# Kernel tuning notes

Measured on AMD Instinct MI355X. Metric: run time of the kernel, lower is better.

Reference implementation:

```python
import jax, jax.numpy as jnp
import numpy as np

QK_I2_S = 128  # weights per block; 32 packed bytes per block
RMS_EPS = 1e-6  # RMSNorm default eps (BitNetMLP builds RMSNorm without eps arg)


def unpack_simd(packed, K):
    """Unpack SIMD block-interleaved 2-bit weights to float {-1,0,1,2}-1 values.

    packed: [M, K//4] uint8. Within each 128-weight block (32 bytes):
      byte[j] bits 6:7 -> w[j+0], 4:5 -> w[j+32], 2:3 -> w[j+64], 0:1 -> w[j+96].
    """
    M = packed.shape[0]
    nb = K // QK_I2_S
    b = packed.astype(jnp.int32).reshape(M, nb, 32)
    # stack shift groups so flattened order is [j+0..31, j+32.., j+64.., j+96..]
    w = jnp.stack([(b >> 6) & 3, (b >> 4) & 3, (b >> 2) & 3, b & 3], axis=2)  # [M,nb,4,32]
    return w.reshape(M, K).astype(jnp.float32) - 1.0


def setup_inputs() -> dict:
    key = jax.random.key(0)
    ks = jax.random.split(key, 8)
    H, I = 2560, 6912
    B, S = 4, 2048
    x = jax.random.normal(ks[0], (B, S, H), dtype=jnp.float32)
    gate_packed = jax.random.randint(ks[1], (I, H // 4), 0, 256, dtype=jnp.int32).astype(jnp.uint8)
    up_packed = jax.random.randint(ks[2], (I, H // 4), 0, 256, dtype=jnp.int32).astype(jnp.uint8)
    down_packed = jax.random.randint(ks[3], (H, I // 4), 0, 256, dtype=jnp.int32).astype(jnp.uint8)
    gate_scale = jax.random.uniform(ks[4], (1,), minval=0.01, maxval=0.1, dtype=jnp.float32)
    up_scale = jax.random.uniform(ks[5], (1,), minval=0.01, maxval=0.1, dtype=jnp.float32)
    down_scale = jax.random.uniform(ks[6], (1,), minval=0.01, maxval=0.1, dtype=jnp.float32)
    norm_w = jnp.ones((I,), dtype=jnp.float32) + 0.05 * jax.random.normal(ks[7], (I,), dtype=jnp.float32)
    return {"x": x, "gate_packed": gate_packed, "gate_scale": gate_scale,
            "up_packed": up_packed, "up_scale": up_scale,
            "down_packed": down_packed, "down_scale": down_scale,
            "norm_w": norm_w}


def reference(x, gate_packed, gate_scale, up_packed, up_scale, down_packed, down_scale, norm_w):
    H = x.shape[-1]
    I = norm_w.shape[0]
    # BitLinear (fallback path math): unpack ternary weights, apply scalar weight scale
    Wg = unpack_simd(gate_packed, H) * gate_scale[0]   # [I, H]
    Wu = unpack_simd(up_packed, H) * up_scale[0]       # [I, H]
    Wd = unpack_simd(down_packed, I) * down_scale[0]   # [H, I]
    gate = jnp.einsum('bsh,ih->bsi', x, Wg)
    up = jnp.einsum('bsh,ih->bsi', x, Wu)
    hidden = jnp.square(jax.nn.relu(gate)) * up        # ReLU^2 gating
    # RMSNorm over intermediate dim
    var = jnp.mean(jnp.square(hidden), axis=-1, keepdims=True)
    hidden = norm_w * (hidden * jax.lax.rsqrt(var + RMS_EPS))
    return jnp.einsum('bsi,hi->bsh', hidden, Wd)
```

## Files before the change

### kernel.cpp

```cpp
#include <hip/hip_runtime.h>
#include <cstdint>
#include <cstddef>

#define H_DIM 2560
#define I_DIM 6912
#define NTOK  8192

typedef __attribute__((ext_vector_type(8))) __bf16 bf16x8;
typedef __attribute__((ext_vector_type(4))) float  f32x4;

__device__ inline void gld16(void* lds, const void* g) {
    __builtin_amdgcn_global_load_lds(
        (__attribute__((address_space(1))) void*)(void*)g,
        (__attribute__((address_space(3))) void*)lds, 16, 0, 0);
}

__global__ __launch_bounds__(256) void cvt_x_kernel(const float* __restrict__ x,
                                                    __bf16* __restrict__ xb, int n8) {
    int gid = blockIdx.x * 256 + threadIdx.x;
    if (gid >= n8) return;
    const float4* p = (const float4*)(x + (size_t)gid * 8);
    float4 v0 = p[0], v1 = p[1];
    bf16x8 o;
    o[0] = (__bf16)v0.x; o[1] = (__bf16)v0.y; o[2] = (__bf16)v0.z; o[3] = (__bf16)v0.w;
    o[4] = (__bf16)v1.x; o[5] = (__bf16)v1.y; o[6] = (__bf16)v1.z; o[7] = (__bf16)v1.w;
    *(bf16x8*)(xb + (size_t)gid * 8) = o;
}

__global__ __launch_bounds__(256) void unpack_w_kernel(const int* __restrict__ packed,
                                                       __bf16* __restrict__ out,
                                                       int M, int K,
                                                       const float* __restrict__ norm,
                                                       int mode) {
    int gid = blockIdx.x * 256 + threadIdx.x;
    int per_row = K >> 3;
    if (gid >= M * per_row) return;
    int i  = gid / per_row;
    int k0 = (gid % per_row) * 8;
    int blk = k0 >> 7;
    int grp = (k0 >> 5) & 3;
    int j0  = k0 & 31;
    int shift = 6 - 2 * grp;
    const int* p = packed + (size_t)i * (K >> 2) + blk * 32 + j0;
    int4 v0 = *(const int4*)p;
    int4 v1 = *(const int4*)(p + 4);
    int vals[8] = {v0.x, v0.y, v0.z, v0.w, v1.x, v1.y, v1.z, v1.w};
    bf16x8 o;
#pragma unroll
    for (int b = 0; b < 8; ++b) {
        float f = (float)(((vals[b] >> shift) & 3) - 1);
        if (norm) f *= norm[k0 + b];
        o[b] = (__bf16)f;
    }
    int dst = (mode == 0) ? i : ((i >> 4) * 32 + (i & 15) + ((mode == 2) ? 16 : 0));
    *(bf16x8*)(out + (size_t)dst * K + k0) = o;
}

__global__ __launch_bounds__(256) void rms_rs_kernel(const __bf16* __restrict__ hidden,
                                                     float* __restrict__ rs) {
    const int tk = blockIdx.x;
    const __bf16* row = hidden + (size_t)tk * I_DIM;
    float s = 0.f;
    for (int idx = threadIdx.x; idx < I_DIM / 8; idx += 256) {
        bf16x8 v = *(const bf16x8*)&row[idx * 8];
#pragma unroll
        for (int j = 0; j < 8; ++j) { float f = (float)v[j]; s += f * f; }
    }
#pragma unroll
    for (int off = 32; off; off >>= 1) s += __shfl_down(s, off, 64);
    __shared__ float wsum[4];
    if ((threadIdx.x & 63) == 0) wsum[threadIdx.x >> 6] = s;
    __syncthreads();
    if (threadIdx.x == 0) {
        float tot = wsum[0] + wsum[1] + wsum[2] + wsum[3];
        rs[tk] = rsqrtf(tot / (float)I_DIM + 1e-6f);
    }
}

template<int KDIM, bool GATED>
__global__ __launch_bounds__(512) void gemm_pipe(
    const __bf16* __restrict__ A,
    const __bf16* __restrict__ B,
    const float* __restrict__ s0,
    const float* __restrict__ s1,
    const float* __restrict__ rs,
    void* __restrict__ outp,
    int nby)
{
    constexpr int BM = 256, BN = 128, BK = 64;
    constexpr int NT = KDIM / BK;
    constexpr int SLOTB = (BM + BN) * BK * 2;
    __shared__ __align__(16) char smem[3 * SLOTB];

    const int nwg = (int)gridDim.x;
    const int q = nwg >> 3;
    const int id = (int)blockIdx.x;
    const int wg = (id & 7) * q + (id >> 3);
    const int bx = wg / nby;
    const int by = wg % nby;

    const int m0 = bx * BM;
    const int n0 = by * BN;
    const int t  = (int)threadIdx.x;
    const int lane = t & 63;
    const int wm = (t >> 6) >> 1;
    const int wn = (t >> 6) & 1;

    const int srow = t >> 3;
    const int scol = ((t & 7) * 16) ^ ((srow & 7) << 4);
    const char* gA = (const char*)A + (size_t)(m0 + srow) * (KDIM * 2) + scol;
    const char* gB = (const char*)B + (size_t)(n0 + srow) * (KDIM * 2) + scol;
    char* lbase = smem + t * 16;

    const int l15 = lane & 15;
    const int xv  = (l15 & 7) << 4;
    const int colx[2] = { (((lane >> 4) * 16) ^ xv), ((64 + (lane >> 4) * 16) ^ xv) };

    f32x4 acc[4][4];
#pragma unroll
    for (int a = 0; a < 4; ++a)
#pragma unroll
        for (int b = 0; b < 4; ++b) acc[a][b] = (f32x4){0, 0, 0, 0};

#define STAGE_T(s, kt) do {                                                     \
        char* _ls = lbase + (s) * SLOTB;                                        \
        const char* _ga = gA + (kt) * (BK * 2);                                 \
        _Pragma("unroll")                                                       \
        for (int _i = 0; _i < 4; ++_i)                                          \
            gld16(_ls + _i * 8192, _ga + (size_t)_i * 64 * (KDIM * 2));         \
        const char* _gb = gB + (kt) * (BK * 2);                                 \
        char* _lb = _ls + BM * BK * 2;                                          \
        _Pragma("unroll")                                                       \
        for (int _i = 0; _i < 2; ++_i)                                          \
            gld16(_lb + _i * 8192, _gb + (size_t)_i * 64 * (KDIM * 2));         \
    } while (0)

#define COMPUTE_T(s) do {                                                       \
        const char* _sa = smem + (s) * SLOTB;                                   \
        const char* _sb = _sa + BM * BK * 2;                                    \
        _Pragma("unroll")                                                       \
        for (int _kk = 0; _kk < 2; ++_kk) {                                     \
            bf16x8 _a[4], _b[4];                                                \
            _Pragma("unroll")                                                   \
            for (int _f = 0; _f < 4; ++_f)                                      \
                _a[_f] = *(const bf16x8*)(_sa + (wm * 64 + _f * 16 + l15) * 128 + colx[_kk]); \
            _Pragma("unroll")                                                   \
            for (int _f = 0; _f < 4; ++_f)                                      \
                _b[_f] = *(const bf16x8*)(_sb + (wn * 64 + _f * 16 + l15) * 128 + colx[_kk]); \
            __builtin_amdgcn_s_setprio(1);                                      \
            _Pragma("unroll")                                                   \
            for (int _fm = 0; _fm < 4; ++_fm)                                   \
                _Pragma("unroll")                                               \
                for (int _fn = 0; _fn < 4; ++_fn)                               \
                    acc[_fm][_fn] = __builtin_amdgcn_mfma_f32_16x16x32_bf16(    \
                        _a[_fm], _b[_fn], acc[_fm][_fn], 0, 0, 0);              \
            __builtin_amdgcn_s_setprio(0);                                      \
        }                                                                       \
    } while (0)

    STAGE_T(0, 0);
    STAGE_T(1, 1);
    asm volatile("s_waitcnt vmcnt(6)" ::: "memory");
    __builtin_amdgcn_s_barrier();
    asm volatile("" ::: "memory");

    for (int kt = 0; kt < NT; ++kt) {
        if (kt + 2 < NT) STAGE_T((kt + 2) % 3, kt + 2);
        COMPUTE_T(kt % 3);
        if (kt + 2 < NT) {
            asm volatile("s_waitcnt vmcnt(6)" ::: "memory");
            __builtin_amdgcn_s_barrier();
            asm volatile("" ::: "memory");
        } else if (kt + 2 == NT) {
            asm volatile("s_waitcnt vmcnt(0)" ::: "memory");
            __builtin_amdgcn_s_barrier();
            asm volatile("" ::: "memory");
        }
    }

#undef STAGE_T
#undef COMPUTE_T

    const int r0 = m0 + wm * 64 + (lane >> 4) * 4;
    if (GATED) {
        const float comb = s0[0] * s0[0] * s1[0];
        __bf16* hid = (__bf16*)outp;
        const int i0 = by * 64 + wn * 32 + l15;
#pragma unroll
        for (int fm = 0; fm < 4; ++fm)
#pragma unroll
            for (int p = 0; p < 2; ++p)
#pragma unroll
                for (int j = 0; j < 4; ++j) {
                    float g = acc[fm][2 * p][j];
                    float u = acc[fm][2 * p + 1][j];
                    float r = fmaxf(g, 0.f);
                    hid[(size_t)(r0 + fm * 16 + j) * I_DIM + (i0 + p * 16)] =
                        (__bf16)(comb * r * r * u);
                }
    } else {
        const float ds = s0[0];
        float* outf = (float*)outp;
#pragma unroll
        for (int fm = 0; fm < 4; ++fm)
#pragma unroll
            for (int j = 0; j < 4; ++j) {
                const int row = r0 + fm * 16 + j;
                const float sc = ds * rs[row];
#pragma unroll
                for (int fn = 0; fn < 4; ++fn)
                    outf[(size_t)row * H_DIM + (n0 + wn * 64 + fn * 16 + l15)] =
                        sc * acc[fm][fn][j];
            }
    }
}

extern "C" void kernel_launch(void* const* d_in, const int* in_sizes, int n_in,
                              void* d_out, int out_size, void* d_ws, size_t ws_size,
                              hipStream_t stream) {
    const float* x   = (const float*)d_in[0];
    const int*   gp  = (const int*)d_in[1];
    const float* gs  = (const float*)d_in[2];
    const int*   upk = (const int*)d_in[3];
    const float* us  = (const float*)d_in[4];
    const int*   dp  = (const int*)d_in[5];
    const float* dsc = (const float*)d_in[6];
    const float* nw  = (const float*)d_in[7];
    float* out = (float*)d_out;

    char* ws = (char*)d_ws;
    __bf16* xb     = (__bf16*)ws;  ws += (size_t)NTOK * H_DIM * 2;
    __bf16* bgu    = (__bf16*)ws;  ws += (size_t)2 * I_DIM * H_DIM * 2;
    __bf16* wdb    = (__bf16*)ws;  ws += (size_t)H_DIM * I_DIM * 2;
    __bf16* hidden = (__bf16*)ws;  ws += (size_t)NTOK * I_DIM * 2;
    float*  rsbuf  = (float*)ws;   ws += (size_t)NTOK * 4;

    cvt_x_kernel<<<(NTOK * H_DIM / 8 + 255) / 256, 256, 0, stream>>>(x, xb, NTOK * H_DIM / 8);
    unpack_w_kernel<<<(I_DIM * H_DIM / 8 + 255) / 256, 256, 0, stream>>>(gp, bgu, I_DIM, H_DIM, nullptr, 1);
    unpack_w_kernel<<<(I_DIM * H_DIM / 8 + 255) / 256, 256, 0, stream>>>(upk, bgu, I_DIM, H_DIM, nullptr, 2);
    unpack_w_kernel<<<(H_DIM * I_DIM / 8 + 255) / 256, 256, 0, stream>>>(dp, wdb, H_DIM, I_DIM, nw, 0);

    gemm_pipe<H_DIM, true><<<dim3((NTOK / 256) * (2 * I_DIM / 128)), 512, 0, stream>>>(
        xb, bgu, gs, us, nullptr, hidden, 2 * I_DIM / 128);

    rms_rs_kernel<<<NTOK, 256, 0, stream>>>(hidden, rsbuf);

    gemm_pipe<I_DIM, false><<<dim3((NTOK / 256) * (H_DIM / 128)), 512, 0, stream>>>(
        hidden, wdb, dsc, nullptr, rsbuf, out, H_DIM / 128);
}
```

Measured before the change: 941.2 us.

## Use 256x256 tiled gate/up GEMM with double-buffered interleaved LDS staging

Replaces the generic gated GEMM with a dedicated kernel that uses a 256x256 output tile (8x4 MFMA fragments per wave). It double-buffers 128KB of LDS, interleaves half-tile global-to-LDS loads with MFMA phases, and raises wave priority around the MFMA groups. The larger tile is meant to cut global/L2 traffic per FLOP and improve the MFMA-to-load ratio. In exchange it uses more accumulator registers and one workgroup of LDS per CU, and the sync schedule is more complex. The down-projection GEMM is split out unchanged.

New measurement: 855.4 us. 1.1x faster.

```diff
diff --git a/kernel.cpp b/kernel.cpp
--- a/kernel.cpp
+++ b/kernel.cpp
@@ -77,14 +77,142 @@
     }
 }
 
-template<int KDIM, bool GATED>
-__global__ __launch_bounds__(512) void gemm_pipe(
+template<int KDIM>
+__global__ __launch_bounds__(512, 2) void gemm_gu8(
     const __bf16* __restrict__ A,
     const __bf16* __restrict__ B,
-    const float* __restrict__ s0,
-    const float* __restrict__ s1,
+    const float* __restrict__ gs_p,
+    const float* __restrict__ us_p,
+    __bf16* __restrict__ hidden,
+    int nby)
+{
+    constexpr int KB = KDIM * 2;
+    constexpr int NT = KDIM / 64;
+    __shared__ __align__(16) char smem[131072];
+
+    const int nwg = (int)gridDim.x;
+    const int q = nwg >> 3;
+    const int id = (int)blockIdx.x;
+    const int wg = (id & 7) * q + (id >> 3);
+    const int bx = wg / nby, by = wg % nby;
+    const int m0 = bx * 256, n0 = by * 256;
+
+    const int t = (int)threadIdx.x;
+    const int lane = t & 63;
+    const int wid = t >> 6;
+    const int wm = wid >> 2, wn = wid & 3;
+    const int l15 = lane & 15, s8 = lane >> 4;
+
+    const int qa  = (t & 7) ^ ((t >> 3) & 7);
+    const int rA2 = ((t >> 3) << 1) + (qa >> 2);
+    const char* gA0 = (const char*)A + (size_t)(m0 + rA2) * KB + (qa & 3) * 16;
+    const char* gA1 = (const char*)A + (size_t)(m0 + 128 + rA2) * KB + (qa & 3) * 16;
+    const int sr0 = t >> 3, sr1 = 64 + (t >> 3);
+    const int br0 = ((sr0 >> 5) << 6) + (sr0 & 31);
+    const int br1 = ((sr1 >> 5) << 6) + (sr1 & 31);
+    const char* gB0 = (const char*)B + (size_t)(n0 + br0) * KB + qa * 16;
+    const char* gB1 = (const char*)B + (size_t)(n0 + br1) * KB + qa * 16;
+    char* ldst = smem + t * 16;
+
+    const int aoff = (wm * 64 + (l15 >> 1)) * 128 +
+                     (((((l15 & 1) << 2) | s8) ^ ((l15 >> 1) & 7)) << 4);
+    const int boff = (wn * 32 + l15) * 128;
+    const int bco0 = ((s8) ^ (l15 & 7)) << 4;
+    const int bco1 = ((4 | s8) ^ (l15 & 7)) << 4;
+
+    f32x4 acc[8][4];
+#pragma unroll
+    for (int f = 0; f < 8; ++f)
+#pragma unroll
+        for (int n = 0; n < 4; ++n) acc[f][n] = (f32x4){0, 0, 0, 0};
+
+#define STG_A(d, kt, kk) do {                                              \
+        size_t _oA = (size_t)(kt) * 128 + (kk) * 64;                       \
+        gld16(ldst + (d) * 65536 + (kk) * 16384,        gA0 + _oA);        \
+        gld16(ldst + (d) * 65536 + (kk) * 16384 + 8192, gA1 + _oA);        \
+    } while (0)
+#define STG_B(d, kt, nh) do {                                              \
+        size_t _oB = (size_t)(nh) * 32 * KB + (size_t)(kt) * 128;          \
+        gld16(ldst + (d) * 65536 + 32768 + (nh) * 16384,        gB0 + _oB);\
+        gld16(ldst + (d) * 65536 + 32768 + (nh) * 16384 + 8192, gB1 + _oB);\
+    } while (0)
+#define LOAD_A(d, kk) do { _Pragma("unroll")                               \
+        for (int _f = 0; _f < 8; ++_f)                                     \
+            a[_f] = *(const bf16x8*)(smem + (d) * 65536 + (kk) * 16384 +   \
+                                     _f * 1024 + aoff); } while (0)
+#define LOAD_B(d, nh, bc) do {                                             \
+        b0 = *(const bf16x8*)(smem + (d) * 65536 + 32768 + (nh) * 16384 +  \
+                              boff + (bc));                                \
+        b1 = *(const bf16x8*)(smem + (d) * 65536 + 32768 + (nh) * 16384 +  \
+                              boff + (bc) + 2048); } while (0)
+#define MFMA16(nh) do { __builtin_amdgcn_s_setprio(1); _Pragma("unroll")   \
+        for (int _f = 0; _f < 8; ++_f) {                                   \
+            acc[_f][(nh) * 2] = __builtin_amdgcn_mfma_f32_16x16x32_bf16(   \
+                a[_f], b0, acc[_f][(nh) * 2], 0, 0, 0);                    \
+            acc[_f][(nh) * 2 + 1] = __builtin_amdgcn_mfma_f32_16x16x32_bf16(\
+                a[_f], b1, acc[_f][(nh) * 2 + 1], 0, 0, 0); }              \
+        __builtin_amdgcn_s_setprio(0); } while (0)
+#define BAR() do { asm volatile("" ::: "memory");                          \
+        __builtin_amdgcn_s_barrier();                                      \
+        asm volatile("" ::: "memory"); } while (0)
+
+    STG_A(0, 0, 0); STG_A(0, 0, 1); STG_B(0, 0, 0); STG_B(0, 0, 1);
+    STG_A(1, 1, 0); STG_B(1, 1, 0);
+    asm volatile("s_waitcnt vmcnt(4)" ::: "memory");
+    BAR();
+
+    bf16x8 a[8], b0, b1;
+    for (int kt = 0; kt < NT; ++kt) {
+        const int d = kt & 1;
+        LOAD_A(d, 0); LOAD_B(d, 0, bco0);
+        if (kt + 1 < NT) STG_A(d ^ 1, kt + 1, 1);
+        BAR(); MFMA16(0); BAR();
+        LOAD_B(d, 1, bco0);
+        if (kt + 1 < NT) STG_B(d ^ 1, kt + 1, 1);
+        BAR(); MFMA16(1); BAR();
+        LOAD_A(d, 1); LOAD_B(d, 0, bco1);
+        if (kt + 2 < NT) STG_A(d, kt + 2, 0);
+        BAR(); MFMA16(0); BAR();
+        LOAD_B(d, 1, bco1);
+        if (kt + 2 < NT) {
+            STG_B(d, kt + 2, 0);
+            asm volatile("s_waitcnt vmcnt(4)" ::: "memory");
+        } else {
+            asm volatile("s_waitcnt vmcnt(0)" ::: "memory");
+        }
+        BAR(); MFMA16(1); BAR();
+    }
+
+#undef STG_A
+#undef STG_B
+#undef LOAD_A
+#undef LOAD_B
+#undef MFMA16
+#undef BAR
+
+    const float comb = gs_p[0] * gs_p[0] * us_p[0];
+    const int r0 = m0 + wm * 128 + s8 * 4;
+#pragma unroll
+    for (int f = 0; f < 8; ++f)
+#pragma unroll
+        for (int p = 0; p < 2; ++p)
+#pragma unroll
+            for (int j = 0; j < 4; ++j) {
+                float g = acc[f][2 * p][j];
+                float u = acc[f][2 * p + 1][j];
+                float r = fmaxf(g, 0.f);
+                hidden[(size_t)(r0 + f * 16 + j) * I_DIM +
+                       ((by * 8 + wn * 2 + p) * 16 + l15)] = (__bf16)(comb * r * r * u);
+            }
+}
+
+template<int KDIM>
+__global__ __launch_bounds__(512) void gemm_down_pipe(
+    const __bf16* __restrict__ A,
+    const __bf16* __restrict__ B,
+    const float* __restrict__ ds_p,
     const float* __restrict__ rs,
-    void* __restrict__ outp,
+    float* __restrict__ outf,
     int nby)
 {
     constexpr int BM = 256, BN = 128, BK = 64;
@@ -181,38 +309,19 @@
 #undef STAGE_T
 #undef COMPUTE_T
 
+    const float ds = ds_p[0];
     const int r0 = m0 + wm * 64 + (lane >> 4) * 4;
-    if (GATED) {
-        const float comb = s0[0] * s0[0] * s1[0];
-        __bf16* hid = (__bf16*)outp;
-        const int i0 = by * 64 + wn * 32 + l15;
-#pragma unroll
-        for (int fm = 0; fm < 4; ++fm)
-#pragma unroll
-            for (int p = 0; p < 2; ++p)
-#pragma unroll
-                for (int j = 0; j < 4; ++j) {
-                    float g = acc[fm][2 * p][j];
-                    float u = acc[fm][2 * p + 1][j];
-                    float r = fmaxf(g, 0.f);
-                    hid[(size_t)(r0 + fm * 16 + j) * I_DIM + (i0 + p * 16)] =
-                        (__bf16)(comb * r * r * u);
-                }
-    } else {
-        const float ds = s0[0];
-        float* outf = (float*)outp;
-#pragma unroll
-        for (int fm = 0; fm < 4; ++fm)
-#pragma unroll
-            for (int j = 0; j < 4; ++j) {
-                const int row = r0 + fm * 16 + j;
-                const float sc = ds * rs[row];
-#pragma unroll
-                for (int fn = 0; fn < 4; ++fn)
-                    outf[(size_t)row * H_DIM + (n0 + wn * 64 + fn * 16 + l15)] =
-                        sc * acc[fm][fn][j];
-            }
-    }
+#pragma unroll
+    for (int fm = 0; fm < 4; ++fm)
+#pragma unroll
+        for (int j = 0; j < 4; ++j) {
+            const int row = r0 + fm * 16 + j;
+            const float sc = ds * rs[row];
+#pragma unroll
+            for (int fn = 0; fn < 4; ++fn)
+                outf[(size_t)row * H_DIM + (n0 + wn * 64 + fn * 16 + l15)] =
+                    sc * acc[fm][fn][j];
+        }
 }
 
 extern "C" void kernel_launch(void* const* d_in, const int* in_sizes, int n_in,
@@ -240,11 +349,11 @@
     unpack_w_kernel<<<(I_DIM * H_DIM / 8 + 255) / 256, 256, 0, stream>>>(upk, bgu, I_DIM, H_DIM, nullptr, 2);
     unpack_w_kernel<<<(H_DIM * I_DIM / 8 + 255) / 256, 256, 0, stream>>>(dp, wdb, H_DIM, I_DIM, nw, 0);
 
-    gemm_pipe<H_DIM, true><<<dim3((NTOK / 256) * (2 * I_DIM / 128)), 512, 0, stream>>>(
-        xb, bgu, gs, us, nullptr, hidden, 2 * I_DIM / 128);
+    gemm_gu8<H_DIM><<<dim3((NTOK / 256) * (2 * I_DIM / 256)), 512, 0, stream>>>(
+        xb, bgu, gs, us, hidden, 2 * I_DIM / 256);
 
     rms_rs_kernel<<<NTOK, 256, 0, stream>>>(hidden, rsbuf);
 
-    gemm_pipe<I_DIM, false><<<dim3((NTOK / 256) * (H_DIM / 128)), 512, 0, stream>>>(
-        hidden, wdb, dsc, nullptr, rsbuf, out, H_DIM / 128);
-}
+    gemm_down_pipe<I_DIM><<<dim3((NTOK / 256) * (H_DIM / 128)), 512, 0, stream>>>(
+        hidden, wdb, dsc, rsbuf, out, H_DIM / 128);
+}
```
